# Performance work log

Measured on AMD Instinct MI355X. Metric: run time of the kernel, lower is better.

## Reference

```python
import jax, jax.numpy as jnp
import numpy as np

N, E = 50000, 800000
F_IN, F_EDGE = 64, 16
HEADS, C_HEAD = 4, 32
HC = HEADS * C_HEAD  # 128 = hidden_node_channels
MLP_IN = F_IN + HC   # 192
MLP0, MLP1 = 128, 128
NEG_SLOPE = 0.2


def leaky_relu(x):
    return jnp.where(x >= 0, x, NEG_SLOPE * x)


def layer_norm(x, g, b, eps=1e-5):
    mu = jnp.mean(x, axis=-1, keepdims=True)
    var = jnp.mean(jnp.square(x - mu), axis=-1, keepdims=True)
    return (x - mu) * jax.lax.rsqrt(var + eps) * g + b


def setup_inputs() -> dict:
    key = jax.random.key(0)
    ks = jax.random.split(key, 24)
    s = 0.05
    inp = {
        "node_features": jax.random.normal(ks[0], (N, F_IN), jnp.float32),
        "edge_features": jax.random.normal(ks[1], (E, F_EDGE), jnp.float32),
        "edge_index": jax.random.randint(ks[2], (2, E), 0, N, jnp.int32),
        # GATv2Conv params (share_weights=False, bias=True, edge_dim=16)
        "W_l": jax.random.normal(ks[3], (F_IN, HC), jnp.float32) * s,
        "b_l": jax.random.normal(ks[4], (HC,), jnp.float32) * s,
        "W_r": jax.random.normal(ks[5], (F_IN, HC), jnp.float32) * s,
        "b_r": jax.random.normal(ks[6], (HC,), jnp.float32) * s,
        "W_e": jax.random.normal(ks[7], (F_EDGE, HC), jnp.float32) * s,
        "att": jax.random.normal(ks[8], (HEADS, C_HEAD), jnp.float32) * s,
        "gat_bias": jax.random.normal(ks[9], (HC,), jnp.float32) * s,
        # residual_connection: Linear(64->128) + LayerNorm
        "res_W": jax.random.normal(ks[10], (F_IN, MLP1), jnp.float32) * s,
        "res_b": jax.random.normal(ks[11], (MLP1,), jnp.float32) * s,
        "res_g": 1.0 + jax.random.normal(ks[12], (MLP1,), jnp.float32) * s,
        "res_beta": jax.random.normal(ks[13], (MLP1,), jnp.float32) * s,
        # upd MLP: two ffn_blocks (Linear -> LayerNorm -> ReLU)
        "W0": jax.random.normal(ks[14], (MLP_IN, MLP0), jnp.float32) * s,
        "b0": jax.random.normal(ks[15], (MLP0,), jnp.float32) * s,
        "g0": 1.0 + jax.random.normal(ks[16], (MLP0,), jnp.float32) * s,
        "beta0": jax.random.normal(ks[17], (MLP0,), jnp.float32) * s,
        "W1": jax.random.normal(ks[18], (MLP0, MLP1), jnp.float32) * s,
        "b1": jax.random.normal(ks[19], (MLP1,), jnp.float32) * s,
        "g1": 1.0 + jax.random.normal(ks[20], (MLP1,), jnp.float32) * s,
        "beta1": jax.random.normal(ks[21], (MLP1,), jnp.float32) * s,
    }
    return inp


def reference(node_features, edge_features, edge_index,
              W_l, b_l, W_r, b_r, W_e, att, gat_bias,
              res_W, res_b, res_g, res_beta,
              W0, b0, g0, beta0, W1, b1, g1, beta1):
    src, dst = edge_index[0], edge_index[1]

    # ---- GATv2Conv ----
    x_l = (node_features @ W_l + b_l).reshape(N, HEADS, C_HEAD)  # source transform
    x_r = (node_features @ W_r + b_r).reshape(N, HEADS, C_HEAD)  # target transform
    e = (edge_features @ W_e).reshape(E, HEADS, C_HEAD)

    x_j = x_l[src]                      # [E,H,C] messages
    m = x_j + x_r[dst] + e              # [E,H,C]
    logits = jnp.sum(leaky_relu(m) * att, axis=-1)  # [E,H]

    # segment softmax over incoming edges of each destination node
    mx = jax.ops.segment_max(logits, dst, num_segments=N)      # [N,H]
    ex = jnp.exp(logits - mx[dst])                             # [E,H]
    den = jax.ops.segment_sum(ex, dst, num_segments=N)         # [N,H]
    alpha = ex / den[dst]                                      # [E,H]

    agg = jax.ops.segment_sum(alpha[..., None] * x_j, dst, num_segments=N)
    gat_out = agg.reshape(N, HC) + gat_bias                    # [N,128]

    # ---- residual concat-MLP ----
    identity = layer_norm(node_features @ res_W + res_b, res_g, res_beta)
    h = jnp.concatenate([node_features, gat_out], axis=-1)     # [N,192]
    h = jax.nn.relu(layer_norm(h @ W0 + b0, g0, beta0))
    h = jax.nn.relu(layer_norm(h @ W1 + b1, g1, beta1))
    return identity + h
```

## Files before the change

kernel.cpp:

```cpp
#include <hip/hip_runtime.h>

#define NN 50000
#define NE 800000
#define NB 196
#define K1B 782

typedef __attribute__((ext_vector_type(8))) short bf16x8;
typedef __attribute__((ext_vector_type(4))) float f32x4;
typedef __attribute__((ext_vector_type(2))) _Float16 h2f;

__device__ __forceinline__ int rfl(int v) { return __builtin_amdgcn_readfirstlane(v); }

__device__ __forceinline__ unsigned short bfb(float x) {
    union { float f; unsigned u; } v; v.f = x;
    unsigned r = v.u + 0x7FFFu + ((v.u >> 16) & 1u);
    return (unsigned short)(r >> 16);
}
__device__ __forceinline__ unsigned pkbf(float lo, float hi) {
    return ((unsigned)bfb(hi) << 16) | (unsigned)bfb(lo);
}
__device__ __forceinline__ unsigned pkh2(float a, float b) {
    union { h2f h; unsigned u; } x;
    x.h.x = (_Float16)a; x.h.y = (_Float16)b;
    return x.u;
}
__device__ __forceinline__ float fdot2u(unsigned a, unsigned b, float c) {
    union { unsigned u; h2f h; } ua, ub; ua.u = a; ub.u = b;
    return __builtin_amdgcn_fdot2(ua.h, ub.h, c, false);
}

__device__ __forceinline__ float dpp_reduce16(float p) {
    int t;
    t = __builtin_amdgcn_update_dpp(0, __float_as_int(p), 0xB1, 0xF, 0xF, false);
    p += __int_as_float(t);
    t = __builtin_amdgcn_update_dpp(0, __float_as_int(p), 0x4E, 0xF, 0xF, false);
    p += __int_as_float(t);
    t = __builtin_amdgcn_update_dpp(0, __float_as_int(p), 0x124, 0xF, 0xF, false);
    p += __int_as_float(t);
    t = __builtin_amdgcn_update_dpp(0, __float_as_int(p), 0x128, 0xF, 0xF, false);
    p += __int_as_float(t);
    return p;
}

__device__ __forceinline__ float exp2_hw(float x) {
    float r;
    asm("v_exp_f32 %0, %1" : "=v"(r) : "v"(x));
    return r;
}

__global__ __launch_bounds__(256) void k0_prep(
    const float* __restrict__ W_l, const float* __restrict__ W_r,
    const float* __restrict__ res_W, const float* __restrict__ W0,
    const float* __restrict__ W1, const float* __restrict__ W_e,
    const float* __restrict__ ef,
    unsigned short* __restrict__ Wtl, unsigned short* __restrict__ Wtr,
    unsigned short* __restrict__ Wtres, unsigned short* __restrict__ Wt0,
    unsigned short* __restrict__ Wt1,
    unsigned* __restrict__ Wep, unsigned* __restrict__ efp,
    int* __restrict__ deg, int* __restrict__ row_start)
{
    const int t0 = blockIdx.x * 256 + threadIdx.x;
    const int nth = gridDim.x * 256;
    for (int t = t0; t < NE * 8; t += nth) {
        float2 v = *(const float2*)(ef + 2 * t);
        efp[t] = pkh2(v.x, v.y);
    }
    if (t0 < 24576) { int n = t0 / 192, k = t0 - n * 192; Wt0[t0] = bfb(W0[k * 128 + n]); }
    if (t0 < 16384) { int n = t0 >> 7, k = t0 & 127; Wt1[t0] = bfb(W1[k * 128 + n]); }
    if (t0 < 8192) {
        int n = t0 >> 6, k = t0 & 63;
        Wtl[t0]   = bfb(W_l[k * 128 + n]);
        Wtr[t0]   = bfb(W_r[k * 128 + n]);
        Wtres[t0] = bfb(res_W[k * 128 + n]);
    }
    if (t0 < 1024) {
        int c = t0 >> 3, j = t0 & 7;
        Wep[t0] = pkh2(W_e[(2 * j) * 128 + c], W_e[(2 * j + 1) * 128 + c]);
    }
    if (t0 < NN) deg[t0] = 0;
    if (t0 == 0) row_start[NN] = NE;
}

__global__ __launch_bounds__(256, 4) void ka_nodes_degree(
    const float* __restrict__ nf,
    const unsigned short* __restrict__ Wtl, const float* __restrict__ b_l,
    const unsigned short* __restrict__ Wtr, const float* __restrict__ b_r,
    const unsigned short* __restrict__ Wtres, const float* __restrict__ res_b,
    const float* __restrict__ res_g, const float* __restrict__ res_beta,
    unsigned* __restrict__ xlp, float* __restrict__ x_r, float* __restrict__ ident,
    const int* __restrict__ eidx, int* __restrict__ deg, int* __restrict__ rank)
{
    if (blockIdx.x >= K1B) {
        int e = (blockIdx.x - K1B) * 256 + threadIdx.x;
        if (e < NE) rank[e] = atomicAdd(deg + eidx[NE + e], 1);
        return;
    }
    __shared__ __align__(16) unsigned As32[64 * 36];
    const int tid = threadIdx.x;
    const int node0 = blockIdx.x * 64;

    for (int i = tid; i < 64 * 32; i += 256) {
        int n = i >> 5, c2 = i & 31;
        int gn = node0 + n;
        float2 v = make_float2(0.f, 0.f);
        if (gn < NN) v = *(const float2*)(nf + gn * 64 + 2 * c2);
        As32[n * 36 + c2] = pkbf(v.x, v.y);
    }
    __syncthreads();

    const int lane = tid & 63, w = tid >> 6;
    const int c = lane & 15, ko = lane >> 4;
    const unsigned short* As = (const unsigned short*)As32;
    bf16x8 a0 = *(const bf16x8*)(As + (w * 16 + c) * 72 + 0 * 32 + ko * 8);
    bf16x8 a1 = *(const bf16x8*)(As + (w * 16 + c) * 72 + 1 * 32 + ko * 8);
    const int lrow0 = node0 + w * 16 + 4 * ko;

    #pragma unroll
    for (int p = 0; p < 3; ++p) {
        const unsigned short* Wt = (p == 0) ? Wtl : (p == 1) ? Wtr : Wtres;
        f32x4 acc[8];
        #pragma unroll
        for (int nt = 0; nt < 8; ++nt) acc[nt] = f32x4{0.f, 0.f, 0.f, 0.f};
        #pragma unroll
        for (int nt = 0; nt < 8; ++nt) {
            bf16x8 bf0 = *(const bf16x8*)(Wt + (nt * 16 + c) * 64 + 0 * 32 + ko * 8);
            acc[nt] = __builtin_amdgcn_mfma_f32_16x16x32_bf16(a0, bf0, acc[nt], 0, 0, 0);
            bf16x8 bf1 = *(const bf16x8*)(Wt + (nt * 16 + c) * 64 + 1 * 32 + ko * 8);
            acc[nt] = __builtin_amdgcn_mfma_f32_16x16x32_bf16(a1, bf1, acc[nt], 0, 0, 0);
        }
        if (p == 0) {
            float bv[8];
            #pragma unroll
            for (int nt = 0; nt < 8; ++nt) bv[nt] = b_l[nt * 16 + c];
            #pragma unroll
            for (int reg = 0; reg < 4; ++reg) {
                int row = lrow0 + reg;
                #pragma unroll
                for (int nt = 0; nt < 8; ++nt) {
                    float v = acc[nt][reg] + bv[nt];
                    float v2 = __shfl_xor(v, 1, 64);
                    if (row < NN && (lane & 1) == 0)
                        xlp[row * 64 + nt * 8 + (c >> 1)] = pkh2(v, v2);
                }
            }
        } else if (p == 1) {
            float bv[8];
            #pragma unroll
            for (int nt = 0; nt < 8; ++nt) bv[nt] = b_r[nt * 16 + c];
            #pragma unroll
            for (int reg = 0; reg < 4; ++reg) {
                int row = lrow0 + reg;
                if (row < NN) {
                    #pragma unroll
                    for (int nt = 0; nt < 8; ++nt)
                        x_r[row * 128 + nt * 16 + c] = acc[nt][reg] + bv[nt];
                }
            }
        } else {
            float bv[8], gv[8], tv[8];
            #pragma unroll
            for (int nt = 0; nt < 8; ++nt) {
                bv[nt] = res_b[nt * 16 + c];
                gv[nt] = res_g[nt * 16 + c];
                tv[nt] = res_beta[nt * 16 + c];
            }
            #pragma unroll
            for (int reg = 0; reg < 4; ++reg) {
                float sum = 0.f, sq = 0.f, hv[8];
                #pragma unroll
                for (int nt = 0; nt < 8; ++nt) {
                    float v = acc[nt][reg] + bv[nt];
                    hv[nt] = v; sum += v; sq += v * v;
                }
                #pragma unroll
                for (int m = 1; m <= 8; m <<= 1) {
                    sum += __shfl_xor(sum, m, 64);
                    sq  += __shfl_xor(sq, m, 64);
                }
                float mean = sum * (1.f / 128.f);
                float inv  = rsqrtf(sq * (1.f / 128.f) - mean * mean + 1e-5f);
                int row = lrow0 + reg;
                if (row < NN) {
                    #pragma unroll
                    for (int nt = 0; nt < 8; ++nt)
                        ident[row * 128 + nt * 16 + c] =
                            (hv[nt] - mean) * inv * gv[nt] + tv[nt];
                }
            }
        }
    }
}

__global__ __launch_bounds__(256) void k3a_blocksum(
    const int* __restrict__ deg, int* __restrict__ bsum)
{
    __shared__ int ws[4];
    int i = blockIdx.x * 256 + threadIdx.x;
    int v = (i < NN) ? deg[i] : 0;
    #pragma unroll
    for (int m = 32; m >= 1; m >>= 1) v += __shfl_xor(v, m, 64);
    if ((threadIdx.x & 63) == 0) ws[threadIdx.x >> 6] = v;
    __syncthreads();
    if (threadIdx.x == 0) bsum[blockIdx.x] = ws[0] + ws[1] + ws[2] + ws[3];
}

__global__ __launch_bounds__(256) void k3c_apply(
    const int* __restrict__ deg, const int* __restrict__ bsum,
    int* __restrict__ row_start)
{
    __shared__ int wsum[4];
    __shared__ int roff[4];
    const int tid = threadIdx.x, lane = tid & 63, wid = tid >> 6;
    int bv = (tid < blockIdx.x) ? bsum[tid] : 0;
    #pragma unroll
    for (int m = 32; m >= 1; m >>= 1) bv += __shfl_xor(bv, m, 64);
    if (lane == 0) roff[wid] = bv;

    int i = blockIdx.x * 256 + tid;
    int v = (i < NN) ? deg[i] : 0;
    int sc = v;
    #pragma unroll
    for (int m = 1; m < 64; m <<= 1) {
        int t = __shfl_up(sc, m, 64);
        if (lane >= m) sc += t;
    }
    if (lane == 63) wsum[wid] = sc;
    __syncthreads();
    int off = roff[0] + roff[1] + roff[2] + roff[3];
    for (int w = 0; w < wid; ++w) off += wsum[w];
    int excl = off + sc - v;
    if (i < NN) row_start[i] = excl;
}

__global__ __launch_bounds__(256) void k4_scatter(
    const int* __restrict__ eidx, const int* __restrict__ row_start,
    const int* __restrict__ rank, int2* __restrict__ csr_es)
{
    int e = blockIdx.x * 256 + threadIdx.x;
    if (e >= NE) return;
    int dst = eidx[NE + e];
    csr_es[row_start[dst] + rank[e]] = make_int2(e, eidx[e]);
}

__global__ __launch_bounds__(256, 4) void k5_attn_aggregate(
    const int2* __restrict__ csr_es, const int* __restrict__ row_start,
    const unsigned* __restrict__ efp, const unsigned* __restrict__ Wep,
    const float* __restrict__ att,
    const unsigned* __restrict__ xlp, const float* __restrict__ x_r,
    const float* __restrict__ gat_bias,
    float* __restrict__ gat_out)
{
    const int lane = threadIdx.x & 63;
    const int node = (blockIdx.x * 256 + threadIdx.x) >> 6;
    if (node >= NN) return;
    const int c = lane * 2;

    uint4 t0 = *(const uint4*)(Wep + c * 8);
    uint4 t1 = *(const uint4*)(Wep + c * 8 + 4);
    uint4 t2 = *(const uint4*)(Wep + (c + 1) * 8);
    uint4 t3 = *(const uint4*)(Wep + (c + 1) * 8 + 4);
    unsigned wx0 = t0.x, wx1 = t0.y, wx2 = t0.z, wx3 = t0.w;
    unsigned wx4 = t1.x, wx5 = t1.y, wx6 = t1.z, wx7 = t1.w;
    unsigned wy0 = t2.x, wy1 = t2.y, wy2 = t2.z, wy3 = t2.w;
    unsigned wy4 = t3.x, wy5 = t3.y, wy6 = t3.z, wy7 = t3.w;

    const float LOG2E = 1.44269504088896340736f;
    float2 a2 = *(const float2*)(att + c);
    a2.x *= LOG2E; a2.y *= LOG2E;
    const float2 xr = *(const float2*)(x_r + node * 128 + c);
    const uint4* __restrict__ efq = (const uint4*)efp;
    const unsigned* __restrict__ xlc = xlp + lane;

    const int sj  = rfl(row_start[node]);
    const int epj = rfl(row_start[node + 1]);

    float den = 0.f, n0 = 0.f, n1 = 0.f;

    for (int base = sj; base < epj; base += 64) {
        const int cnt = min(64, epj - base);
        int pidx = base + lane; if (pidx > NE - 1) pidx = NE - 1;
        const int2 mc = csr_es[pidx];

        uint4 aE0, aE1, bE0, bE1, cE0, cE1, dE0, dE1;
        unsigned aX, bX, cX, dX;

#define LOADS(E0_, E1_, X_, K_)                                            \
        { int kk = (K_); if (kk >= cnt) kk = cnt - 1;                      \
          int eid  = __builtin_amdgcn_readlane(mc.x, kk);                  \
          int srcn = __builtin_amdgcn_readlane(mc.y, kk);                  \
          E0_ = efq[eid * 2 + 0]; E1_ = efq[eid * 2 + 1];                  \
          X_  = xlc[srcn * 64]; }

#define CONSUME(E0_, E1_, X_)                                              \
        { asm volatile("" : "+v"(wx0), "+v"(wx1), "+v"(wx2), "+v"(wx3),    \
                            "+v"(wx4), "+v"(wx5), "+v"(wx6), "+v"(wx7));   \
          asm volatile("" : "+v"(wy0), "+v"(wy1), "+v"(wy2), "+v"(wy3),    \
                            "+v"(wy4), "+v"(wy5), "+v"(wy6), "+v"(wy7));   \
          union { unsigned u; h2f h; } ux; ux.u = (X_);                    \
          float cx0 = (float)ux.h.x, cx1 = (float)ux.h.y;                  \
          float ax = cx0 + xr.x;                                           \
          float ay = cx1 + xr.y;                                           \
          float bx = 0.f, by = 0.f;                                        \
          ax = fdot2u((E0_).x, wx0, ax);  ay = fdot2u((E0_).x, wy0, ay);   \
          bx = fdot2u((E0_).y, wx1, bx);  by = fdot2u((E0_).y, wy1, by);   \
          ax = fdot2u((E0_).z, wx2, ax);  ay = fdot2u((E0_).z, wy2, ay);   \
          bx = fdot2u((E0_).w, wx3, bx);  by = fdot2u((E0_).w, wy3, by);   \
          ax = fdot2u((E1_).x, wx4, ax);  ay = fdot2u((E1_).x, wy4, ay);   \
          bx = fdot2u((E1_).y, wx5, bx);  by = fdot2u((E1_).y, wy5, by);   \
          ax = fdot2u((E1_).z, wx6, ax);  ay = fdot2u((E1_).z, wy6, ay);   \
          bx = fdot2u((E1_).w, wx7, bx);  by = fdot2u((E1_).w, wy7, by);   \
          float evx = ax + bx;                                             \
          float evy = ay + by;                                             \
          float lx = fmaxf(evx, 0.2f * evx);                               \
          float ly = fmaxf(evy, 0.2f * evy);                               \
          float p = lx * a2.x + ly * a2.y;                                 \
          p = dpp_reduce16(p);                                             \
          float ev = exp2_hw(p);                                           \
          den += ev; n0 += ev * cx0; n1 += ev * cx1; }

        LOADS(aE0, aE1, aX, 0);
        LOADS(bE0, bE1, bX, 1);
        LOADS(cE0, cE1, cX, 2);
        int j = 0;
        while (j + 4 <= cnt) {
            LOADS(dE0, dE1, dX, j + 3);
            CONSUME(aE0, aE1, aX);
            LOADS(aE0, aE1, aX, j + 4);
            CONSUME(bE0, bE1, bX);
            LOADS(bE0, bE1, bX, j + 5);
            CONSUME(cE0, cE1, cX);
            LOADS(cE0, cE1, cX, j + 6);
            CONSUME(dE0, dE1, dX);
            j += 4;
        }
        if (j < cnt)     CONSUME(aE0, aE1, aX);
        if (j + 1 < cnt) CONSUME(bE0, bE1, bX);
        if (j + 2 < cnt) CONSUME(cE0, cE1, cX);
#undef LOADS
#undef CONSUME
    }
    float rden = (den > 0.f) ? (1.f / den) : 0.f;
    float2 gb = *(const float2*)(gat_bias + c);
    float2 o; o.x = n0 * rden + gb.x; o.y = n1 * rden + gb.y;
    *(float2*)(gat_out + node * 128 + c) = o;
}

__global__ __launch_bounds__(256, 4) void k6_mlp_mfma(
    const float* __restrict__ nf, const float* __restrict__ gat,
    const float* __restrict__ ident,
    const unsigned short* __restrict__ Wt0, const float* __restrict__ b0,
    const float* __restrict__ g0, const float* __restrict__ be0,
    const unsigned short* __restrict__ Wt1, const float* __restrict__ b1,
    const float* __restrict__ g1, const float* __restrict__ be1,
    float* __restrict__ out)
{
    __shared__ __align__(16) unsigned LDS[64 * 100];
    const int tid = threadIdx.x;
    const int node0 = blockIdx.x * 64;

    for (int i = tid; i < 64 * 96; i += 256) {
        int n = i / 96, c2 = i - n * 96;
        int gn = node0 + n;
        float2 v = make_float2(0.f, 0.f);
        if (gn < NN)
            v = (c2 < 32) ? *(const float2*)(nf + gn * 64 + 2 * c2)
                          : *(const float2*)(gat + gn * 128 + 2 * (c2 - 32));
        LDS[n * 100 + c2] = pkbf(v.x, v.y);
    }
    __syncthreads();

    const int lane = tid & 63, w = tid >> 6;
    const int c = lane & 15, ko = lane >> 4;
    const int lrow = w * 16 + 4 * ko;

    f32x4 acc[8];
    #pragma unroll
    for (int nt = 0; nt < 8; ++nt) acc[nt] = f32x4{0.f, 0.f, 0.f, 0.f};

    #pragma unroll
    for (int kb = 0; kb < 6; ++kb) {
        bf16x8 a = *(const bf16x8*)((const unsigned short*)LDS +
                                    (w * 16 + c) * 200 + kb * 32 + ko * 8);
        #pragma unroll
        for (int nt = 0; nt < 8; ++nt) {
            bf16x8 b = *(const bf16x8*)(Wt0 + (nt * 16 + c) * 192 + kb * 32 + ko * 8);
            acc[nt] = __builtin_amdgcn_mfma_f32_16x16x32_bf16(a, b, acc[nt], 0, 0, 0);
        }
    }

    float bv[8], gv[8], tv[8];
    #pragma unroll
    for (int nt = 0; nt < 8; ++nt) {
        bv[nt] = b0[nt * 16 + c];
        gv[nt] = g0[nt * 16 + c];
        tv[nt] = be0[nt * 16 + c];
    }
    __syncthreads();

    unsigned short* Hs = (unsigned short*)LDS;
    #pragma unroll
    for (int reg = 0; reg < 4; ++reg) {
        float sum = 0.f, sq = 0.f, hv[8];
        #pragma unroll
        for (int nt = 0; nt < 8; ++nt) {
            float v = acc[nt][reg] + bv[nt];
            hv[nt] = v; sum += v; sq += v * v;
        }
        #pragma unroll
        for (int m = 1; m <= 8; m <<= 1) {
            sum += __shfl_xor(sum, m, 64);
            sq  += __shfl_xor(sq, m, 64);
        }
        float mean = sum * (1.f / 128.f);
        float inv  = rsqrtf(sq * (1.f / 128.f) - mean * mean + 1e-5f);
        #pragma unroll
        for (int nt = 0; nt < 8; ++nt) {
            float h = fmaxf((hv[nt] - mean) * inv * gv[nt] + tv[nt], 0.f);
            Hs[(lrow + reg) * 136 + nt * 16 + c] = bfb(h);
        }
    }
    __syncthreads();

    #pragma unroll
    for (int nt = 0; nt < 8; ++nt) acc[nt] = f32x4{0.f, 0.f, 0.f, 0.f};
    #pragma unroll
    for (int kb = 0; kb < 4; ++kb) {
        bf16x8 a = *(const bf16x8*)((const unsigned short*)LDS +
                                    (w * 16 + c) * 136 + kb * 32 + ko * 8);
        #pragma unroll
        for (int nt = 0; nt < 8; ++nt) {
            bf16x8 b = *(const bf16x8*)(Wt1 + (nt * 16 + c) * 128 + kb * 32 + ko * 8);
            acc[nt] = __builtin_amdgcn_mfma_f32_16x16x32_bf16(a, b, acc[nt], 0, 0, 0);
        }
    }

    #pragma unroll
    for (int nt = 0; nt < 8; ++nt) {
        bv[nt] = b1[nt * 16 + c];
        gv[nt] = g1[nt * 16 + c];
        tv[nt] = be1[nt * 16 + c];
    }
    #pragma unroll
    for (int reg = 0; reg < 4; ++reg) {
        float sum = 0.f, sq = 0.f, hv[8];
        #pragma unroll
        for (int nt = 0; nt < 8; ++nt) {
            float v = acc[nt][reg] + bv[nt];
            hv[nt] = v; sum += v; sq += v * v;
        }
        #pragma unroll
        for (int m = 1; m <= 8; m <<= 1) {
            sum += __shfl_xor(sum, m, 64);
            sq  += __shfl_xor(sq, m, 64);
        }
        float mean = sum * (1.f / 128.f);
        float inv  = rsqrtf(sq * (1.f / 128.f) - mean * mean + 1e-5f);
        int row = node0 + lrow + reg;
        if (row < NN) {
            #pragma unroll
            for (int nt = 0; nt < 8; ++nt) {
                float h = fmaxf((hv[nt] - mean) * inv * gv[nt] + tv[nt], 0.f);
                int col = nt * 16 + c;
                out[row * 128 + col] = ident[row * 128 + col] + h;
            }
        }
    }
}

extern "C" void kernel_launch(void* const* d_in, const int* in_sizes, int n_in,
                              void* d_out, int out_size, void* d_ws, size_t ws_size,
                              hipStream_t stream)
{
    const float* nf       = (const float*)d_in[0];
    const float* ef       = (const float*)d_in[1];
    const int*   eidx     = (const int*)d_in[2];
    const float* W_l      = (const float*)d_in[3];
    const float* b_l      = (const float*)d_in[4];
    const float* W_r      = (const float*)d_in[5];
    const float* b_r      = (const float*)d_in[6];
    const float* W_e      = (const float*)d_in[7];
    const float* att      = (const float*)d_in[8];
    const float* gat_bias = (const float*)d_in[9];
    const float* res_W    = (const float*)d_in[10];
    const float* res_b    = (const float*)d_in[11];
    const float* res_g    = (const float*)d_in[12];
    const float* res_beta = (const float*)d_in[13];
    const float* W0       = (const float*)d_in[14];
    const float* b0       = (const float*)d_in[15];
    const float* g0       = (const float*)d_in[16];
    const float* beta0    = (const float*)d_in[17];
    const float* W1       = (const float*)d_in[18];
    const float* b1       = (const float*)d_in[19];
    const float* g1       = (const float*)d_in[20];
    const float* beta1    = (const float*)d_in[21];
    float* out = (float*)d_out;

    char* ws = (char*)d_ws;
    size_t off = 0;
    auto alloc = [&](size_t bytes) -> void* {
        void* p = ws + off;
        off += (bytes + 255) & ~(size_t)255;
        return p;
    };
    unsigned* xlp  = (unsigned*)alloc((size_t)NN * 64 * 4);
    float* x_r     = (float*)alloc((size_t)NN * 128 * 4);
    float* ident   = (float*)alloc((size_t)NN * 128 * 4);
    int* deg       = (int*)alloc((size_t)NN * 4);
    int* row_start = (int*)alloc((size_t)(NN + 1) * 4);
    int* rank      = (int*)alloc((size_t)NE * 4);
    int* bsum      = (int*)alloc((size_t)(NB + 1) * 4);
    int2* csr_es   = (int2*)alloc((size_t)NE * 8);
    float* gat_out = (float*)alloc((size_t)NN * 128 * 4);
    unsigned short* Wtl   = (unsigned short*)alloc(8192 * 2);
    unsigned short* Wtr   = (unsigned short*)alloc(8192 * 2);
    unsigned short* Wtres = (unsigned short*)alloc(8192 * 2);
    unsigned short* Wt0   = (unsigned short*)alloc(24576 * 2);
    unsigned short* Wt1   = (unsigned short*)alloc(16384 * 2);
    unsigned* Wep = (unsigned*)alloc(1024 * 4);
    unsigned* efp = (unsigned*)alloc((size_t)NE * 8 * 4);

    k0_prep<<<8192, 256, 0, stream>>>(W_l, W_r, res_W, W0, W1, W_e, ef,
                                      Wtl, Wtr, Wtres, Wt0, Wt1, Wep, efp,
                                      deg, row_start);

    ka_nodes_degree<<<K1B + (NE + 255) / 256, 256, 0, stream>>>(
        nf, Wtl, b_l, Wtr, b_r, Wtres, res_b, res_g, res_beta,
        xlp, x_r, ident, eidx, deg, rank);

    k3a_blocksum<<<NB, 256, 0, stream>>>(deg, bsum);
    k3c_apply<<<NB, 256, 0, stream>>>(deg, bsum, row_start);

    k4_scatter<<<(NE + 255) / 256, 256, 0, stream>>>(eidx, row_start, rank, csr_es);

    k5_attn_aggregate<<<(NN * 64 + 255) / 256, 256, 0, stream>>>(
        csr_es, row_start, efp, Wep, att, xlp, x_r, gat_bias, gat_out);

    k6_mlp_mfma<<<(NN + 63) / 64, 256, 0, stream>>>(
        nf, gat_out, ident, Wt0, b0, g0, beta0, Wt1, b1, g1, beta1, out);
}
```

Measured before the change: 336.1 us.

## Pack edge features in CSR order and deepen attention prefetch pipeline

Replaces the per-edge packed feature array with one permuted into CSR order by a new kernel, so the attention kernel reads edge features contiguously instead of gathering by edge id. The attention loop prefetch depth grows from 4 to 6 edges. The DPP reduction is rewritten as fused DPP adds in inline assembly to remove separate move instructions. The new packing kernel does a random gather itself and adds an extra launch. The inline assembly may bypass compiler hazard handling for DPP.

```diff
diff --git a/kernel.cpp b/kernel.cpp
--- a/kernel.cpp
+++ b/kernel.cpp
@@ -30,15 +30,14 @@
 }
 
 __device__ __forceinline__ float dpp_reduce16(float p) {
-    int t;
-    t = __builtin_amdgcn_update_dpp(0, __float_as_int(p), 0xB1, 0xF, 0xF, false);
-    p += __int_as_float(t);
-    t = __builtin_amdgcn_update_dpp(0, __float_as_int(p), 0x4E, 0xF, 0xF, false);
-    p += __int_as_float(t);
-    t = __builtin_amdgcn_update_dpp(0, __float_as_int(p), 0x124, 0xF, 0xF, false);
-    p += __int_as_float(t);
-    t = __builtin_amdgcn_update_dpp(0, __float_as_int(p), 0x128, 0xF, 0xF, false);
-    p += __int_as_float(t);
+    asm("v_add_f32 %0, %0, %0 quad_perm:[1,0,3,2] row_mask:0xf bank_mask:0xf"
+        : "+v"(p));
+    asm("v_add_f32 %0, %0, %0 quad_perm:[2,3,0,1] row_mask:0xf bank_mask:0xf"
+        : "+v"(p));
+    asm("v_add_f32 %0, %0, %0 row_ror:4 row_mask:0xf bank_mask:0xf"
+        : "+v"(p));
+    asm("v_add_f32 %0, %0, %0 row_ror:8 row_mask:0xf bank_mask:0xf"
+        : "+v"(p));
     return p;
 }
 
@@ -52,19 +51,13 @@
     const float* __restrict__ W_l, const float* __restrict__ W_r,
     const float* __restrict__ res_W, const float* __restrict__ W0,
     const float* __restrict__ W1, const float* __restrict__ W_e,
-    const float* __restrict__ ef,
     unsigned short* __restrict__ Wtl, unsigned short* __restrict__ Wtr,
     unsigned short* __restrict__ Wtres, unsigned short* __restrict__ Wt0,
     unsigned short* __restrict__ Wt1,
-    unsigned* __restrict__ Wep, unsigned* __restrict__ efp,
+    unsigned* __restrict__ Wep,
     int* __restrict__ deg, int* __restrict__ row_start)
 {
     const int t0 = blockIdx.x * 256 + threadIdx.x;
-    const int nth = gridDim.x * 256;
-    for (int t = t0; t < NE * 8; t += nth) {
-        float2 v = *(const float2*)(ef + 2 * t);
-        efp[t] = pkh2(v.x, v.y);
-    }
     if (t0 < 24576) { int n = t0 / 192, k = t0 - n * 192; Wt0[t0] = bfb(W0[k * 128 + n]); }
     if (t0 < 16384) { int n = t0 >> 7, k = t0 & 127; Wt1[t0] = bfb(W1[k * 128 + n]); }
     if (t0 < 8192) {
@@ -242,9 +235,27 @@
     csr_es[row_start[dst] + rank[e]] = make_int2(e, eidx[e]);
 }
 
+__global__ __launch_bounds__(256) void k4b_efpack(
+    const int2* __restrict__ csr_es, const float* __restrict__ ef,
+    unsigned* __restrict__ csr_ef)
+{
+    int p = blockIdx.x * 256 + threadIdx.x;
+    if (p >= NE) return;
+    int eid = csr_es[p].x;
+    const float4* efr = (const float4*)(ef + (size_t)eid * 16);
+    float4 v0 = efr[0], v1 = efr[1], v2 = efr[2], v3 = efr[3];
+    uint4 o0, o1;
+    o0.x = pkh2(v0.x, v0.y); o0.y = pkh2(v0.z, v0.w);
+    o0.z = pkh2(v1.x, v1.y); o0.w = pkh2(v1.z, v1.w);
+    o1.x = pkh2(v2.x, v2.y); o1.y = pkh2(v2.z, v2.w);
+    o1.z = pkh2(v3.x, v3.y); o1.w = pkh2(v3.z, v3.w);
+    *(uint4*)(csr_ef + (size_t)p * 8)     = o0;
+    *(uint4*)(csr_ef + (size_t)p * 8 + 4) = o1;
+}
+
 __global__ __launch_bounds__(256, 4) void k5_attn_aggregate(
     const int2* __restrict__ csr_es, const int* __restrict__ row_start,
-    const unsigned* __restrict__ efp, const unsigned* __restrict__ Wep,
+    const unsigned* __restrict__ csr_ef, const unsigned* __restrict__ Wep,
     const float* __restrict__ att,
     const unsigned* __restrict__ xlp, const float* __restrict__ x_r,
     const float* __restrict__ gat_bias,
@@ -268,7 +279,7 @@
     float2 a2 = *(const float2*)(att + c);
     a2.x *= LOG2E; a2.y *= LOG2E;
     const float2 xr = *(const float2*)(x_r + node * 128 + c);
-    const uint4* __restrict__ efq = (const uint4*)efp;
+    const uint4* __restrict__ cef = (const uint4*)csr_ef;
     const unsigned* __restrict__ xlc = xlp + lane;
 
     const int sj  = rfl(row_start[node]);
@@ -281,14 +292,14 @@
         int pidx = base + lane; if (pidx > NE - 1) pidx = NE - 1;
         const int2 mc = csr_es[pidx];
 
-        uint4 aE0, aE1, bE0, bE1, cE0, cE1, dE0, dE1;
-        unsigned aX, bX, cX, dX;
+        uint4 aE0, aE1, bE0, bE1, cE0, cE1, dE0, dE1, eE0, eE1, fE0, fE1;
+        unsigned aX, bX, cX, dX, eX, fX;
 
 #define LOADS(E0_, E1_, X_, K_)                                            \
         { int kk = (K_); if (kk >= cnt) kk = cnt - 1;                      \
-          int eid  = __builtin_amdgcn_readlane(mc.x, kk);                  \
           int srcn = __builtin_amdgcn_readlane(mc.y, kk);                  \
-          E0_ = efq[eid * 2 + 0]; E1_ = efq[eid * 2 + 1];                  \
+          int ep = (base + kk) * 2;                                        \
+          E0_ = cef[ep]; E1_ = cef[ep + 1];                                \
           X_  = xlc[srcn * 64]; }
 
 #define CONSUME(E0_, E1_, X_)                                              \
@@ -321,21 +332,29 @@
         LOADS(aE0, aE1, aX, 0);
         LOADS(bE0, bE1, bX, 1);
         LOADS(cE0, cE1, cX, 2);
+        LOADS(dE0, dE1, dX, 3);
+        LOADS(eE0, eE1, eX, 4);
         int j = 0;
-        while (j + 4 <= cnt) {
-            LOADS(dE0, dE1, dX, j + 3);
+        while (j + 6 <= cnt) {
+            LOADS(fE0, fE1, fX, j + 5);
             CONSUME(aE0, aE1, aX);
-            LOADS(aE0, aE1, aX, j + 4);
+            LOADS(aE0, aE1, aX, j + 6);
             CONSUME(bE0, bE1, bX);
-            LOADS(bE0, bE1, bX, j + 5);
+            LOADS(bE0, bE1, bX, j + 7);
             CONSUME(cE0, cE1, cX);
-            LOADS(cE0, cE1, cX, j + 6);
+            LOADS(cE0, cE1, cX, j + 8);
             CONSUME(dE0, dE1, dX);
-            j += 4;
+            LOADS(dE0, dE1, dX, j + 9);
+            CONSUME(eE0, eE1, eX);
+            LOADS(eE0, eE1, eX, j + 10);
+            CONSUME(fE0, fE1, fX);
+            j += 6;
         }
         if (j < cnt)     CONSUME(aE0, aE1, aX);
         if (j + 1 < cnt) CONSUME(bE0, bE1, bX);
         if (j + 2 < cnt) CONSUME(cE0, cE1, cX);
+        if (j + 3 < cnt) CONSUME(dE0, dE1, dX);
+        if (j + 4 < cnt) CONSUME(eE0, eE1, eX);
 #undef LOADS
 #undef CONSUME
     }
@@ -510,6 +529,7 @@
     int* rank      = (int*)alloc((size_t)NE * 4);
     int* bsum      = (int*)alloc((size_t)(NB + 1) * 4);
     int2* csr_es   = (int2*)alloc((size_t)NE * 8);
+    unsigned* csr_ef = (unsigned*)alloc((size_t)NE * 8 * 4);
     float* gat_out = (float*)alloc((size_t)NN * 128 * 4);
     unsigned short* Wtl   = (unsigned short*)alloc(8192 * 2);
     unsigned short* Wtr   = (unsigned short*)alloc(8192 * 2);
@@ -517,11 +537,10 @@
     unsigned short* Wt0   = (unsigned short*)alloc(24576 * 2);
     unsigned short* Wt1   = (unsigned short*)alloc(16384 * 2);
     unsigned* Wep = (unsigned*)alloc(1024 * 4);
-    unsigned* efp = (unsigned*)alloc((size_t)NE * 8 * 4);
-
-    k0_prep<<<8192, 256, 0, stream>>>(W_l, W_r, res_W, W0, W1, W_e, ef,
-                                      Wtl, Wtr, Wtres, Wt0, Wt1, Wep, efp,
-                                      deg, row_start);
+
+    k0_prep<<<NB, 256, 0, stream>>>(W_l, W_r, res_W, W0, W1, W_e,
+                                    Wtl, Wtr, Wtres, Wt0, Wt1, Wep,
+                                    deg, row_start);
 
     ka_nodes_degree<<<K1B + (NE + 255) / 256, 256, 0, stream>>>(
         nf, Wtl, b_l, Wtr, b_r, Wtres, res_b, res_g, res_beta,
@@ -532,8 +551,10 @@
 
     k4_scatter<<<(NE + 255) / 256, 256, 0, stream>>>(eidx, row_start, rank, csr_es);
 
+    k4b_efpack<<<(NE + 255) / 256, 256, 0, stream>>>(csr_es, ef, csr_ef);
+
     k5_attn_aggregate<<<(NN * 64 + 255) / 256, 256, 0, stream>>>(
-        csr_es, row_start, efp, Wep, att, xlp, x_r, gat_bias, gat_out);
+        csr_es, row_start, csr_ef, Wep, att, xlp, x_r, gat_bias, gat_out);
 
     k6_mlp_mfma<<<(NN + 63) / 64, 256, 0, stream>>>(
         nf, gat_out, ident, Wt0, b0, g0, beta0, Wt1, b1, g1, beta1, out);
```

After: 349.2 us. +3.9%, slower.

## Compute per-edge projection with MFMA in attention kernel, drop edge-feature prepack

Applied to the files above, without the earlier changes.

The attention/aggregation kernel now processes edges in groups of 16 and computes the edge-feature projection (16->128) with f16 MFMA 16x16x32 instead of per-lane fdot2 chains. The wave is re-laid out so each lane owns 8 channels for 4 edges, and the DPP reduction becomes a quad reduction followed by cross-row shuffles at the end. The fp32 edge features are read and converted to f16 inside the kernel, so the separate prepack pass over all edges in the prep kernel is removed and that kernel shrinks to a small grid. Occupancy hint drops to 3 waves per EU, and half of the lanes load zeros for the unused K padding of the MFMA.

```diff
diff --git a/kernel.cpp b/kernel.cpp
--- a/kernel.cpp
+++ b/kernel.cpp
@@ -8,6 +8,7 @@
 typedef __attribute__((ext_vector_type(8))) short bf16x8;
 typedef __attribute__((ext_vector_type(4))) float f32x4;
 typedef __attribute__((ext_vector_type(2))) _Float16 h2f;
+typedef __attribute__((ext_vector_type(8))) _Float16 f16x8v;
 
 __device__ __forceinline__ int rfl(int v) { return __builtin_amdgcn_readfirstlane(v); }
 
@@ -24,22 +25,8 @@
     x.h.x = (_Float16)a; x.h.y = (_Float16)b;
     return x.u;
 }
-__device__ __forceinline__ float fdot2u(unsigned a, unsigned b, float c) {
-    union { unsigned u; h2f h; } ua, ub; ua.u = a; ub.u = b;
-    return __builtin_amdgcn_fdot2(ua.h, ub.h, c, false);
-}
-
-__device__ __forceinline__ float dpp_reduce16(float p) {
-    int t;
-    t = __builtin_amdgcn_update_dpp(0, __float_as_int(p), 0xB1, 0xF, 0xF, false);
-    p += __int_as_float(t);
-    t = __builtin_amdgcn_update_dpp(0, __float_as_int(p), 0x4E, 0xF, 0xF, false);
-    p += __int_as_float(t);
-    t = __builtin_amdgcn_update_dpp(0, __float_as_int(p), 0x124, 0xF, 0xF, false);
-    p += __int_as_float(t);
-    t = __builtin_amdgcn_update_dpp(0, __float_as_int(p), 0x128, 0xF, 0xF, false);
-    p += __int_as_float(t);
-    return p;
+__device__ __forceinline__ unsigned short h16(float x) {
+    union { _Float16 h; unsigned short s; } u; u.h = (_Float16)x; return u.s;
 }
 
 __device__ __forceinline__ float exp2_hw(float x) {
@@ -52,19 +39,13 @@
     const float* __restrict__ W_l, const float* __restrict__ W_r,
     const float* __restrict__ res_W, const float* __restrict__ W0,
     const float* __restrict__ W1, const float* __restrict__ W_e,
-    const float* __restrict__ ef,
     unsigned short* __restrict__ Wtl, unsigned short* __restrict__ Wtr,
     unsigned short* __restrict__ Wtres, unsigned short* __restrict__ Wt0,
     unsigned short* __restrict__ Wt1,
-    unsigned* __restrict__ Wep, unsigned* __restrict__ efp,
+    unsigned short* __restrict__ Wef,
     int* __restrict__ deg, int* __restrict__ row_start)
 {
     const int t0 = blockIdx.x * 256 + threadIdx.x;
-    const int nth = gridDim.x * 256;
-    for (int t = t0; t < NE * 8; t += nth) {
-        float2 v = *(const float2*)(ef + 2 * t);
-        efp[t] = pkh2(v.x, v.y);
-    }
     if (t0 < 24576) { int n = t0 / 192, k = t0 - n * 192; Wt0[t0] = bfb(W0[k * 128 + n]); }
     if (t0 < 16384) { int n = t0 >> 7, k = t0 & 127; Wt1[t0] = bfb(W1[k * 128 + n]); }
     if (t0 < 8192) {
@@ -73,9 +54,9 @@
         Wtr[t0]   = bfb(W_r[k * 128 + n]);
         Wtres[t0] = bfb(res_W[k * 128 + n]);
     }
-    if (t0 < 1024) {
-        int c = t0 >> 3, j = t0 & 7;
-        Wep[t0] = pkh2(W_e[(2 * j) * 128 + c], W_e[(2 * j + 1) * 128 + c]);
+    if (t0 < 2048) {
+        int ch = t0 >> 4, k = t0 & 15;
+        Wef[t0] = h16(W_e[k * 128 + ch]);
     }
     if (t0 < NN) deg[t0] = 0;
     if (t0 == 0) row_start[NN] = NE;
@@ -242,9 +223,9 @@
     csr_es[row_start[dst] + rank[e]] = make_int2(e, eidx[e]);
 }
 
-__global__ __launch_bounds__(256, 4) void k5_attn_aggregate(
+__global__ __launch_bounds__(256, 3) void k5_attn_aggregate(
     const int2* __restrict__ csr_es, const int* __restrict__ row_start,
-    const unsigned* __restrict__ efp, const unsigned* __restrict__ Wep,
+    const float* __restrict__ ef, const unsigned short* __restrict__ Wef,
     const float* __restrict__ att,
     const unsigned* __restrict__ xlp, const float* __restrict__ x_r,
     const float* __restrict__ gat_bias,
@@ -253,96 +234,129 @@
     const int lane = threadIdx.x & 63;
     const int node = (blockIdx.x * 256 + threadIdx.x) >> 6;
     if (node >= NN) return;
-    const int c = lane * 2;
-
-    uint4 t0 = *(const uint4*)(Wep + c * 8);
-    uint4 t1 = *(const uint4*)(Wep + c * 8 + 4);
-    uint4 t2 = *(const uint4*)(Wep + (c + 1) * 8);
-    uint4 t3 = *(const uint4*)(Wep + (c + 1) * 8 + 4);
-    unsigned wx0 = t0.x, wx1 = t0.y, wx2 = t0.z, wx3 = t0.w;
-    unsigned wx4 = t1.x, wx5 = t1.y, wx6 = t1.z, wx7 = t1.w;
-    unsigned wy0 = t2.x, wy1 = t2.y, wy2 = t2.z, wy3 = t2.w;
-    unsigned wy4 = t3.x, wy5 = t3.y, wy6 = t3.z, wy7 = t3.w;
+    const int cq = lane & 15;
+    const int ko = lane >> 4;
+    const int q4 = ko * 4;
+    const int ch0 = cq * 8;
+    const bool kok = ko < 2;
+
+    union BU { uint4 u; f16x8v h; };
+    f16x8v B[8];
+    #pragma unroll
+    for (int t = 0; t < 8; ++t) {
+        BU b; b.u = make_uint4(0u, 0u, 0u, 0u);
+        if (kok) b.u = *(const uint4*)(Wef + (ch0 + t) * 16 + ko * 8);
+        B[t] = b.h;
+    }
 
     const float LOG2E = 1.44269504088896340736f;
-    float2 a2 = *(const float2*)(att + c);
-    a2.x *= LOG2E; a2.y *= LOG2E;
-    const float2 xr = *(const float2*)(x_r + node * 128 + c);
-    const uint4* __restrict__ efq = (const uint4*)efp;
-    const unsigned* __restrict__ xlc = xlp + lane;
+    float attv[8], xrv[8];
+    {
+        float4 a0 = *(const float4*)(att + ch0);
+        float4 a1 = *(const float4*)(att + ch0 + 4);
+        attv[0] = a0.x * LOG2E; attv[1] = a0.y * LOG2E;
+        attv[2] = a0.z * LOG2E; attv[3] = a0.w * LOG2E;
+        attv[4] = a1.x * LOG2E; attv[5] = a1.y * LOG2E;
+        attv[6] = a1.z * LOG2E; attv[7] = a1.w * LOG2E;
+        float4 x0 = *(const float4*)(x_r + node * 128 + ch0);
+        float4 x1 = *(const float4*)(x_r + node * 128 + ch0 + 4);
+        xrv[0] = x0.x; xrv[1] = x0.y; xrv[2] = x0.z; xrv[3] = x0.w;
+        xrv[4] = x1.x; xrv[5] = x1.y; xrv[6] = x1.z; xrv[7] = x1.w;
+    }
 
     const int sj  = rfl(row_start[node]);
     const int epj = rfl(row_start[node + 1]);
-
-    float den = 0.f, n0 = 0.f, n1 = 0.f;
+    const unsigned short* __restrict__ xlus = (const unsigned short*)xlp;
+
+    float den = 0.f;
+    float n[8];
+    #pragma unroll
+    for (int t = 0; t < 8; ++t) n[t] = 0.f;
+
+    union XU { uint4 u; _Float16 h[8]; };
 
     for (int base = sj; base < epj; base += 64) {
         const int cnt = min(64, epj - base);
-        int pidx = base + lane; if (pidx > NE - 1) pidx = NE - 1;
+        int pidx = base + lane;
+        const int pmax = epj - 1;
+        if (pidx > pmax) pidx = pmax;
         const int2 mc = csr_es[pidx];
-
-        uint4 aE0, aE1, bE0, bE1, cE0, cE1, dE0, dE1;
-        unsigned aX, bX, cX, dX;
-
-#define LOADS(E0_, E1_, X_, K_)                                            \
-        { int kk = (K_); if (kk >= cnt) kk = cnt - 1;                      \
-          int eid  = __builtin_amdgcn_readlane(mc.x, kk);                  \
-          int srcn = __builtin_amdgcn_readlane(mc.y, kk);                  \
-          E0_ = efq[eid * 2 + 0]; E1_ = efq[eid * 2 + 1];                  \
-          X_  = xlc[srcn * 64]; }
-
-#define CONSUME(E0_, E1_, X_)                                              \
-        { asm volatile("" : "+v"(wx0), "+v"(wx1), "+v"(wx2), "+v"(wx3),    \
-                            "+v"(wx4), "+v"(wx5), "+v"(wx6), "+v"(wx7));   \
-          asm volatile("" : "+v"(wy0), "+v"(wy1), "+v"(wy2), "+v"(wy3),    \
-                            "+v"(wy4), "+v"(wy5), "+v"(wy6), "+v"(wy7));   \
-          union { unsigned u; h2f h; } ux; ux.u = (X_);                    \
-          float cx0 = (float)ux.h.x, cx1 = (float)ux.h.y;                  \
-          float ax = cx0 + xr.x;                                           \
-          float ay = cx1 + xr.y;                                           \
-          float bx = 0.f, by = 0.f;                                        \
-          ax = fdot2u((E0_).x, wx0, ax);  ay = fdot2u((E0_).x, wy0, ay);   \
-          bx = fdot2u((E0_).y, wx1, bx);  by = fdot2u((E0_).y, wy1, by);   \
-          ax = fdot2u((E0_).z, wx2, ax);  ay = fdot2u((E0_).z, wy2, ay);   \
-          bx = fdot2u((E0_).w, wx3, bx);  by = fdot2u((E0_).w, wy3, by);   \
-          ax = fdot2u((E1_).x, wx4, ax);  ay = fdot2u((E1_).x, wy4, ay);   \
-          bx = fdot2u((E1_).y, wx5, bx);  by = fdot2u((E1_).y, wy5, by);   \
-          ax = fdot2u((E1_).z, wx6, ax);  ay = fdot2u((E1_).z, wy6, ay);   \
-          bx = fdot2u((E1_).w, wx7, bx);  by = fdot2u((E1_).w, wy7, by);   \
-          float evx = ax + bx;                                             \
-          float evy = ay + by;                                             \
-          float lx = fmaxf(evx, 0.2f * evx);                               \
-          float ly = fmaxf(evy, 0.2f * evy);                               \
-          float p = lx * a2.x + ly * a2.y;                                 \
-          p = dpp_reduce16(p);                                             \
-          float ev = exp2_hw(p);                                           \
-          den += ev; n0 += ev * cx0; n1 += ev * cx1; }
-
-        LOADS(aE0, aE1, aX, 0);
-        LOADS(bE0, bE1, bX, 1);
-        LOADS(cE0, cE1, cX, 2);
-        int j = 0;
-        while (j + 4 <= cnt) {
-            LOADS(dE0, dE1, dX, j + 3);
-            CONSUME(aE0, aE1, aX);
-            LOADS(aE0, aE1, aX, j + 4);
-            CONSUME(bE0, bE1, bX);
-            LOADS(bE0, bE1, bX, j + 5);
-            CONSUME(cE0, cE1, cX);
-            LOADS(cE0, cE1, cX, j + 6);
-            CONSUME(dE0, dE1, dX);
-            j += 4;
-        }
-        if (j < cnt)     CONSUME(aE0, aE1, aX);
-        if (j + 1 < cnt) CONSUME(bE0, bE1, bX);
-        if (j + 2 < cnt) CONSUME(cE0, cE1, cX);
-#undef LOADS
-#undef CONSUME
+        const int nb = (cnt + 15) >> 4;
+
+        for (int b = 0; b < nb; ++b) {
+            int eid = __shfl(mc.x, b * 16 + cq, 64);
+            f16x8v A = f16x8v{0, 0, 0, 0, 0, 0, 0, 0};
+            if (kok) {
+                const float4* er = (const float4*)(ef + (size_t)eid * 16 + ko * 8);
+                float4 v0 = er[0], v1 = er[1];
+                A[0] = (_Float16)v0.x; A[1] = (_Float16)v0.y;
+                A[2] = (_Float16)v0.z; A[3] = (_Float16)v0.w;
+                A[4] = (_Float16)v1.x; A[5] = (_Float16)v1.y;
+                A[6] = (_Float16)v1.z; A[7] = (_Float16)v1.w;
+            }
+
+            int s0 = __shfl(mc.y, b * 16 + q4 + 0, 64);
+            int s1 = __shfl(mc.y, b * 16 + q4 + 1, 64);
+            int s2 = __shfl(mc.y, b * 16 + q4 + 2, 64);
+            int s3 = __shfl(mc.y, b * 16 + q4 + 3, 64);
+            XU xa, xb, xc, xd;
+            xa.u = *(const uint4*)(xlus + s0 * 128 + ch0);
+            xb.u = *(const uint4*)(xlus + s1 * 128 + ch0);
+            xc.u = *(const uint4*)(xlus + s2 * 128 + ch0);
+            xd.u = *(const uint4*)(xlus + s3 * 128 + ch0);
+
+            f32x4 acc[8];
+            #pragma unroll
+            for (int t = 0; t < 8; ++t)
+                acc[t] = f32x4{xrv[t], xrv[t], xrv[t], xrv[t]};
+            #pragma unroll
+            for (int t = 0; t < 8; ++t)
+                acc[t] = __builtin_amdgcn_mfma_f32_16x16x32_f16(A, B[t], acc[t], 0, 0, 0);
+
+#define EPI(R, XR)                                                          \
+            { float p = 0.f; float xlv[8];                                  \
+              _Pragma("unroll")                                             \
+              for (int t = 0; t < 8; ++t) {                                 \
+                  float xl = (float)XR.h[t];                                \
+                  xlv[t] = xl;                                              \
+                  float m = acc[t][R] + xl;                                 \
+                  p = fmaf(fmaxf(m, 0.2f * m), attv[t], p);                 \
+              }                                                             \
+              asm("v_add_f32 %0, %0, %0 quad_perm:[1,0,3,2] row_mask:0xf bank_mask:0xf" : "+v"(p)); \
+              asm("v_add_f32 %0, %0, %0 quad_perm:[2,3,0,1] row_mask:0xf bank_mask:0xf" : "+v"(p)); \
+              float ev = exp2_hw(p);                                        \
+              ev = ((b * 16 + q4 + R) < cnt) ? ev : 0.f;                    \
+              den += ev;                                                    \
+              _Pragma("unroll")                                             \
+              for (int t = 0; t < 8; ++t) n[t] = fmaf(ev, xlv[t], n[t]); }
+
+            EPI(0, xa)
+            EPI(1, xb)
+            EPI(2, xc)
+            EPI(3, xd)
+#undef EPI
+        }
+    }
+
+    den += __shfl_xor(den, 16, 64);
+    den += __shfl_xor(den, 32, 64);
+    #pragma unroll
+    for (int t = 0; t < 8; ++t) {
+        n[t] += __shfl_xor(n[t], 16, 64);
+        n[t] += __shfl_xor(n[t], 32, 64);
     }
     float rden = (den > 0.f) ? (1.f / den) : 0.f;
-    float2 gb = *(const float2*)(gat_bias + c);
-    float2 o; o.x = n0 * rden + gb.x; o.y = n1 * rden + gb.y;
-    *(float2*)(gat_out + node * 128 + c) = o;
+    if (lane < 16) {
+        float4 g0 = *(const float4*)(gat_bias + ch0);
+        float4 g1 = *(const float4*)(gat_bias + ch0 + 4);
+        float4 o0, o1;
+        o0.x = fmaf(n[0], rden, g0.x); o0.y = fmaf(n[1], rden, g0.y);
+        o0.z = fmaf(n[2], rden, g0.z); o0.w = fmaf(n[3], rden, g0.w);
+        o1.x = fmaf(n[4], rden, g1.x); o1.y = fmaf(n[5], rden, g1.y);
+        o1.z = fmaf(n[6], rden, g1.z); o1.w = fmaf(n[7], rden, g1.w);
+        *(float4*)(gat_out + node * 128 + ch0)     = o0;
+        *(float4*)(gat_out + node * 128 + ch0 + 4) = o1;
+    }
 }
 
 __global__ __launch_bounds__(256, 4) void k6_mlp_mfma(
@@ -516,12 +530,11 @@
     unsigned short* Wtres = (unsigned short*)alloc(8192 * 2);
     unsigned short* Wt0   = (unsigned short*)alloc(24576 * 2);
     unsigned short* Wt1   = (unsigned short*)alloc(16384 * 2);
-    unsigned* Wep = (unsigned*)alloc(1024 * 4);
-    unsigned* efp = (unsigned*)alloc((size_t)NE * 8 * 4);
-
-    k0_prep<<<8192, 256, 0, stream>>>(W_l, W_r, res_W, W0, W1, W_e, ef,
-                                      Wtl, Wtr, Wtres, Wt0, Wt1, Wep, efp,
-                                      deg, row_start);
+    unsigned short* Wef   = (unsigned short*)alloc(2048 * 2);
+
+    k0_prep<<<NB, 256, 0, stream>>>(W_l, W_r, res_W, W0, W1, W_e,
+                                    Wtl, Wtr, Wtres, Wt0, Wt1, Wef,
+                                    deg, row_start);
 
     ka_nodes_degree<<<K1B + (NE + 255) / 256, 256, 0, stream>>>(
         nf, Wtl, b_l, Wtr, b_r, Wtres, res_b, res_g, res_beta,
@@ -533,7 +546,7 @@
     k4_scatter<<<(NE + 255) / 256, 256, 0, stream>>>(eidx, row_start, rank, csr_es);
 
     k5_attn_aggregate<<<(NN * 64 + 255) / 256, 256, 0, stream>>>(
-        csr_es, row_start, efp, Wep, att, xlp, x_r, gat_bias, gat_out);
+        csr_es, row_start, ef, Wef, att, xlp, x_r, gat_bias, gat_out);
 
     k6_mlp_mfma<<<(NN + 63) / 64, 256, 0, stream>>>(
         nf, gat_out, ident, Wt0, b0, g0, beta0, Wt1, b1, g1, beta1, out);
```

New measurement: 351.5 us. 1.05x slower.

## Fuse edge-feature fp16 packing into degree kernel and deepen gather prefetch to six

Applied to the files above, without the earlier changes.

Moves the conversion of edge features to packed fp16 out of the prep kernel and into the edge-degree branch of the node kernel, one edge per thread with float4 loads. The prep kernel shrinks to NB blocks, which covers only the weight transposes and degree zeroing. This removes a large standalone launch and lets the conversion overlap with the node GEMM blocks. Separately, the attention-aggregate loop's software pipeline is deepened from four to six in-flight edge loads, which hides more gather latency at the cost of more VGPRs and possibly lower occupancy.

```diff
diff --git a/kernel.cpp b/kernel.cpp
--- a/kernel.cpp
+++ b/kernel.cpp
@@ -52,19 +52,13 @@
     const float* __restrict__ W_l, const float* __restrict__ W_r,
     const float* __restrict__ res_W, const float* __restrict__ W0,
     const float* __restrict__ W1, const float* __restrict__ W_e,
-    const float* __restrict__ ef,
     unsigned short* __restrict__ Wtl, unsigned short* __restrict__ Wtr,
     unsigned short* __restrict__ Wtres, unsigned short* __restrict__ Wt0,
     unsigned short* __restrict__ Wt1,
-    unsigned* __restrict__ Wep, unsigned* __restrict__ efp,
+    unsigned* __restrict__ Wep,
     int* __restrict__ deg, int* __restrict__ row_start)
 {
     const int t0 = blockIdx.x * 256 + threadIdx.x;
-    const int nth = gridDim.x * 256;
-    for (int t = t0; t < NE * 8; t += nth) {
-        float2 v = *(const float2*)(ef + 2 * t);
-        efp[t] = pkh2(v.x, v.y);
-    }
     if (t0 < 24576) { int n = t0 / 192, k = t0 - n * 192; Wt0[t0] = bfb(W0[k * 128 + n]); }
     if (t0 < 16384) { int n = t0 >> 7, k = t0 & 127; Wt1[t0] = bfb(W1[k * 128 + n]); }
     if (t0 < 8192) {
@@ -88,11 +82,23 @@
     const unsigned short* __restrict__ Wtres, const float* __restrict__ res_b,
     const float* __restrict__ res_g, const float* __restrict__ res_beta,
     unsigned* __restrict__ xlp, float* __restrict__ x_r, float* __restrict__ ident,
-    const int* __restrict__ eidx, int* __restrict__ deg, int* __restrict__ rank)
+    const int* __restrict__ eidx, int* __restrict__ deg, int* __restrict__ rank,
+    const float* __restrict__ ef, unsigned* __restrict__ efp)
 {
     if (blockIdx.x >= K1B) {
         int e = (blockIdx.x - K1B) * 256 + threadIdx.x;
-        if (e < NE) rank[e] = atomicAdd(deg + eidx[NE + e], 1);
+        if (e < NE) {
+            rank[e] = atomicAdd(deg + eidx[NE + e], 1);
+            const float4* er = (const float4*)(ef + (size_t)e * 16);
+            float4 v0 = er[0], v1 = er[1], v2 = er[2], v3 = er[3];
+            uint4 o0, o1;
+            o0.x = pkh2(v0.x, v0.y); o0.y = pkh2(v0.z, v0.w);
+            o0.z = pkh2(v1.x, v1.y); o0.w = pkh2(v1.z, v1.w);
+            o1.x = pkh2(v2.x, v2.y); o1.y = pkh2(v2.z, v2.w);
+            o1.z = pkh2(v3.x, v3.y); o1.w = pkh2(v3.z, v3.w);
+            *(uint4*)(efp + (size_t)e * 8)     = o0;
+            *(uint4*)(efp + (size_t)e * 8 + 4) = o1;
+        }
         return;
     }
     __shared__ __align__(16) unsigned As32[64 * 36];
@@ -281,8 +287,8 @@
         int pidx = base + lane; if (pidx > NE - 1) pidx = NE - 1;
         const int2 mc = csr_es[pidx];
 
-        uint4 aE0, aE1, bE0, bE1, cE0, cE1, dE0, dE1;
-        unsigned aX, bX, cX, dX;
+        uint4 aE0, aE1, bE0, bE1, cE0, cE1, dE0, dE1, eE0, eE1, fE0, fE1;
+        unsigned aX, bX, cX, dX, eX, fX;
 
 #define LOADS(E0_, E1_, X_, K_)                                            \
         { int kk = (K_); if (kk >= cnt) kk = cnt - 1;                      \
@@ -321,21 +327,29 @@
         LOADS(aE0, aE1, aX, 0);
         LOADS(bE0, bE1, bX, 1);
         LOADS(cE0, cE1, cX, 2);
+        LOADS(dE0, dE1, dX, 3);
+        LOADS(eE0, eE1, eX, 4);
         int j = 0;
-        while (j + 4 <= cnt) {
-            LOADS(dE0, dE1, dX, j + 3);
+        while (j + 6 <= cnt) {
+            LOADS(fE0, fE1, fX, j + 5);
             CONSUME(aE0, aE1, aX);
-            LOADS(aE0, aE1, aX, j + 4);
+            LOADS(aE0, aE1, aX, j + 6);
             CONSUME(bE0, bE1, bX);
-            LOADS(bE0, bE1, bX, j + 5);
+            LOADS(bE0, bE1, bX, j + 7);
             CONSUME(cE0, cE1, cX);
-            LOADS(cE0, cE1, cX, j + 6);
+            LOADS(cE0, cE1, cX, j + 8);
             CONSUME(dE0, dE1, dX);
-            j += 4;
+            LOADS(dE0, dE1, dX, j + 9);
+            CONSUME(eE0, eE1, eX);
+            LOADS(eE0, eE1, eX, j + 10);
+            CONSUME(fE0, fE1, fX);
+            j += 6;
         }
         if (j < cnt)     CONSUME(aE0, aE1, aX);
         if (j + 1 < cnt) CONSUME(bE0, bE1, bX);
         if (j + 2 < cnt) CONSUME(cE0, cE1, cX);
+        if (j + 3 < cnt) CONSUME(dE0, dE1, dX);
+        if (j + 4 < cnt) CONSUME(eE0, eE1, eX);
 #undef LOADS
 #undef CONSUME
     }
@@ -519,13 +533,13 @@
     unsigned* Wep = (unsigned*)alloc(1024 * 4);
     unsigned* efp = (unsigned*)alloc((size_t)NE * 8 * 4);
 
-    k0_prep<<<8192, 256, 0, stream>>>(W_l, W_r, res_W, W0, W1, W_e, ef,
-                                      Wtl, Wtr, Wtres, Wt0, Wt1, Wep, efp,
-                                      deg, row_start);
+    k0_prep<<<NB, 256, 0, stream>>>(W_l, W_r, res_W, W0, W1, W_e,
+                                    Wtl, Wtr, Wtres, Wt0, Wt1, Wep,
+                                    deg, row_start);
 
     ka_nodes_degree<<<K1B + (NE + 255) / 256, 256, 0, stream>>>(
         nf, Wtl, b_l, Wtr, b_r, Wtres, res_b, res_g, res_beta,
-        xlp, x_r, ident, eidx, deg, rank);
+        xlp, x_r, ident, eidx, deg, rank, ef, efp);
 
     k3a_blocksum<<<NB, 256, 0, stream>>>(deg, bsum);
     k3c_apply<<<NB, 256, 0, stream>>>(deg, bsum, row_start);
```

Result: no change. 331.4 us (-1.4%).
